# Performance work log

Measured on AMD Instinct MI355X. Metric: run time of the kernel, lower is better.

## Reference

```python
import jax, jax.numpy as jnp
import numpy as np

EPS = 1e-4  # ReEig clamp


def _spectral(X, f):
    # eigendecompose symmetric X and apply f to eigenvalues: V diag(f(w)) V^T
    w, v = jnp.linalg.eigh(X)
    return jnp.einsum('...ij,...j,...kj->...ik', v, f(w), v)


def _bimap(W, X):
    # W @ X @ W.T with W [out,in], X [b,in,in]
    return jnp.einsum('ij,bjk,lk->bil', W, X, W)


def setup_inputs() -> dict:
    key = jax.random.key(0)
    k1, k2, k3, k4 = jax.random.split(key, 4)
    B = 262144
    vech = jax.random.normal(k1, (B, 6), dtype=jnp.float32)
    # Stiefel init: Q factor of a Gaussian (orthonormal columns)
    W1 = jnp.linalg.qr(jax.random.normal(k2, (5, 3), dtype=jnp.float32))[0]
    W2 = jnp.linalg.qr(jax.random.normal(k3, (7, 5), dtype=jnp.float32))[0]
    W3 = jnp.linalg.qr(jax.random.normal(k4, (9, 7), dtype=jnp.float32))[0]
    return {"vech": vech, "W1": W1, "W2": W2, "W3": W3}


def reference(vech, W1, W2, W3):
    k = 3
    B = vech.shape[0]
    iu = jnp.triu_indices(k)
    X = jnp.zeros((B, k, k), dtype=vech.dtype).at[:, iu[0], iu[1]].set(vech)
    d = jnp.diagonal(X, axis1=-2, axis2=-1)  # [B,3]
    X = X + jnp.swapaxes(X, -2, -1) - d[..., :, None] * jnp.eye(k, dtype=vech.dtype)
    # SPDNet chain
    X = _spectral(X, jnp.exp)                      # ExpEig -> [B,3,3]
    X = _bimap(W1, X)                              # [B,5,5]
    X = _spectral(X, lambda w: jnp.maximum(w, EPS))  # ReEig
    X = _bimap(W2, X)                              # [B,7,7]
    X = _spectral(X, lambda w: jnp.maximum(w, EPS))
    X = _bimap(W3, X)                              # [B,9,9]
    X = _spectral(X, lambda w: jnp.maximum(w, EPS))
    return X
```

## Files before the change

kernel.cpp:

```cpp
#include <hip/hip_runtime.h>

#define EPSV 1e-4f
#define LOG2E 1.4426950408889634f

typedef float v4f __attribute__((ext_vector_type(4)));

__device__ __forceinline__ void jrot(float& app, float& aqq, float& apq,
                                     float& arp, float& arq,
                                     float& vap, float& vaq,
                                     float& vbp, float& vbq,
                                     float& vcp, float& vcq) {
  const float apq0 = apq;
  const float tau = (aqq - app) * (0.5f * __builtin_amdgcn_rcpf(apq0));
  float t = copysignf(
      __builtin_amdgcn_rcpf(fabsf(tau) + sqrtf(fmaf(tau, tau, 1.0f))), tau);
  if (apq0 == 0.0f) t = 0.0f;
  const float c = __builtin_amdgcn_rsqf(fmaf(t, t, 1.0f));
  const float s = t * c;
  const float d = t * apq0;
  app -= d; aqq += d; apq = 0.0f;
  float x, y;
  x = arp; y = arq; arp = fmaf(c, x, -(s * y)); arq = fmaf(s, x, c * y);
  x = vap; y = vaq; vap = fmaf(c, x, -(s * y)); vaq = fmaf(s, x, c * y);
  x = vbp; y = vbq; vbp = fmaf(c, x, -(s * y)); vbq = fmaf(s, x, c * y);
  x = vcp; y = vcq; vcp = fmaf(c, x, -(s * y)); vcq = fmaf(s, x, c * y);
}

__global__ __launch_bounds__(256, 4) void spd_decoder_kernel(
    const float* __restrict__ vech, const float* __restrict__ W1,
    const float* __restrict__ W2, const float* __restrict__ W3,
    float* __restrict__ out, int B) {
  __shared__ float Tsh[21];
  __shared__ float Msh[27];
  __shared__ __align__(16) float buf[4][1296];

  const int tid = threadIdx.x;

  if (tid < 21) {
    const int r = tid / 3, c = tid % 3;
    float acc = 0.f;
#pragma unroll
    for (int j = 0; j < 5; ++j) acc += W2[r * 5 + j] * W1[j * 3 + c];
    Tsh[tid] = acc;
  }
  __syncthreads();
  if (tid < 27) {
    const int r = tid / 3, c = tid % 3;
    float acc = 0.f;
#pragma unroll
    for (int j = 0; j < 7; ++j) acc += W3[r * 7 + j] * Tsh[j * 3 + c];
    Msh[tid] = acc;
  }
  __syncthreads();

  const int e = blockIdx.x * 256 + tid;
  const float2* vp = reinterpret_cast<const float2*>(vech + (size_t)e * 6);
  const float2 p0 = vp[0], p1 = vp[1], p2 = vp[2];
  float a00 = p0.x, a01 = p0.y, a02 = p1.x, a11 = p1.y, a12 = p2.x, a22 = p2.y;

  float v00 = 1.f, v01 = 0.f, v02 = 0.f;
  float v10 = 0.f, v11 = 1.f, v12 = 0.f;
  float v20 = 0.f, v21 = 0.f, v22 = 1.f;
#pragma unroll
  for (int sweep = 0; sweep < 4; ++sweep) {
    jrot(a00, a11, a01, a02, a12, v00, v01, v10, v11, v20, v21);
    jrot(a00, a22, a02, a01, a12, v00, v02, v10, v12, v20, v22);
    jrot(a11, a22, a12, a01, a02, v01, v02, v11, v12, v21, v22);
  }

  const float e0 = exp2f(a00 * LOG2E) - EPSV;
  const float e1 = exp2f(a11 * LOG2E) - EPSV;
  const float e2 = exp2f(a22 * LOG2E) - EPSV;

  float g0[9], g1[9], g2[9];
#pragma unroll
  for (int i = 0; i < 9; ++i) {
    const float m0 = Msh[i * 3 + 0], m1 = Msh[i * 3 + 1], m2 = Msh[i * 3 + 2];
    g0[i] = fmaf(m0, v00, fmaf(m1, v10, m2 * v20));
    g1[i] = fmaf(m0, v01, fmaf(m1, v11, m2 * v21));
    g2[i] = fmaf(m0, v02, fmaf(m1, v12, m2 * v22));
  }

  const int w = tid >> 6, l = tid & 63;
  float* wbuf = &buf[w][0];
  const size_t base = (size_t)(blockIdx.x * 256 + w * 64) * 81;

#pragma unroll
  for (int h = 0; h < 4; ++h) {
    if ((l >> 4) == h) {
      const int ll = l & 15;
      float* dst = wbuf + ll * 81;
#pragma unroll
      for (int i = 0; i < 9; ++i) {
        const float t0 = e0 * g0[i], t1 = e1 * g1[i], t2 = e2 * g2[i];
#pragma unroll
        for (int j = 0; j < 9; ++j) {
          float val = fmaf(t0, g0[j], fmaf(t1, g1[j], t2 * g2[j]));
          if (i == j) val += EPSV;
          dst[i * 9 + j] = val;
        }
      }
    }
    asm volatile("s_waitcnt lgkmcnt(0)" ::: "memory");

    const size_t sb = base + (size_t)h * 1296;
    const v4f* rbuf = reinterpret_cast<const v4f*>(wbuf);
    v4f* outv = reinterpret_cast<v4f*>(out + sb);
#pragma unroll
    for (int it = 0; it < 5; ++it)
      __builtin_nontemporal_store(rbuf[it * 64 + l], outv + it * 64 + l);
    if (l < 4) __builtin_nontemporal_store(rbuf[320 + l], outv + 320 + l);
  }
}

extern "C" void kernel_launch(void* const* d_in, const int* in_sizes, int n_in,
                              void* d_out, int out_size, void* d_ws, size_t ws_size,
                              hipStream_t stream) {
  const float* vech = (const float*)d_in[0];
  const float* W1 = (const float*)d_in[1];
  const float* W2 = (const float*)d_in[2];
  const float* W3 = (const float*)d_in[3];
  float* out = (float*)d_out;
  const int B = in_sizes[0] / 6;
  dim3 grid(B / 256), block(256);
  hipLaunchKernelGGL(spd_decoder_kernel, grid, block, 0, stream,
                     vech, W1, W2, W3, out, B);
}
```

Baseline: 24.65 us.

## Vectorize LDS staging writes, rotate wave store phase, hoist input loads

Each 81-float matrix is written to LDS with 8-byte paired stores, using a parity-dependent shift so every store is aligned even though rows start on odd offsets. This cuts the number of LDS write instructions. The order of the four store phases is now rotated per wave and block to spread global write traffic, and the vech loads are issued before the weight-product setup so their latency overlaps it. The cost is extra select instructions and somewhat more complex indexing.

```diff
diff --git a/kernel.cpp b/kernel.cpp
--- a/kernel.cpp
+++ b/kernel.cpp
@@ -4,6 +4,13 @@
 #define LOG2E 1.4426950408889634f
 
 typedef float v4f __attribute__((ext_vector_type(4)));
+typedef float v2f __attribute__((ext_vector_type(2)));
+
+#define VAL(K)                                                             \
+  (fmaf(e0 * g0[(K) / 9], g0[(K) % 9],                                     \
+        fmaf(e1 * g1[(K) / 9], g1[(K) % 9],                                \
+             (e2 * g2[(K) / 9]) * g2[(K) % 9])) +                          \
+   (((K) / 9 == (K) % 9) ? EPSV : 0.0f))
 
 __device__ __forceinline__ void jrot(float& app, float& aqq, float& apq,
                                      float& arp, float& arq,
@@ -36,6 +43,10 @@
 
   const int tid = threadIdx.x;
 
+  const int e = blockIdx.x * 256 + tid;
+  const float2* vp = reinterpret_cast<const float2*>(vech + (size_t)e * 6);
+  const float2 p0 = vp[0], p1 = vp[1], p2 = vp[2];
+
   if (tid < 21) {
     const int r = tid / 3, c = tid % 3;
     float acc = 0.f;
@@ -53,9 +64,6 @@
   }
   __syncthreads();
 
-  const int e = blockIdx.x * 256 + tid;
-  const float2* vp = reinterpret_cast<const float2*>(vech + (size_t)e * 6);
-  const float2 p0 = vp[0], p1 = vp[1], p2 = vp[2];
   float a00 = p0.x, a01 = p0.y, a02 = p1.x, a11 = p1.y, a12 = p2.x, a22 = p2.y;
 
   float v00 = 1.f, v01 = 0.f, v02 = 0.f;
@@ -84,22 +92,29 @@
   const int w = tid >> 6, l = tid & 63;
   float* wbuf = &buf[w][0];
   const size_t base = (size_t)(blockIdx.x * 256 + w * 64) * 81;
+  const int rot = (w + blockIdx.x) & 3;
 
 #pragma unroll
-  for (int h = 0; h < 4; ++h) {
+  for (int hh = 0; hh < 4; ++hh) {
+    const int h = (hh + rot) & 3;
     if ((l >> 4) == h) {
       const int ll = l & 15;
+      const int d = ll & 1;
       float* dst = wbuf + ll * 81;
+      v2f* pdst = reinterpret_cast<v2f*>(dst + d);
+      const float v0 = VAL(0);
+      float carry = v0;
 #pragma unroll
-      for (int i = 0; i < 9; ++i) {
-        const float t0 = e0 * g0[i], t1 = e1 * g1[i], t2 = e2 * g2[i];
-#pragma unroll
-        for (int j = 0; j < 9; ++j) {
-          float val = fmaf(t0, g0[j], fmaf(t1, g1[j], t2 * g2[j]));
-          if (i == j) val += EPSV;
-          dst[i * 9 + j] = val;
-        }
+      for (int t = 0; t < 40; ++t) {
+        const float vA = VAL(2 * t + 1);
+        const float vB = VAL(2 * t + 2);
+        v2f pv;
+        pv.x = d ? vA : carry;
+        pv.y = d ? vB : vA;
+        pdst[t] = pv;
+        carry = vB;
       }
+      dst[d ? 0 : 80] = d ? v0 : carry;
     }
     asm volatile("s_waitcnt lgkmcnt(0)" ::: "memory");
 
```

New measurement: 25.01 us. No clear change (+1.5%).
